# Kernel optimization log

Measured on AMD Instinct MI355X. Metric: run time of the kernel, lower is better.

Reference implementation:

```python
import jax, jax.numpy as jnp
import numpy as np

B, T, N, H, D = 8, 128, 170, 4, 16
F = H * D  # 64
LN_EPS = 1e-5
MASK_FILL = -(2.0 ** 15) + 1.0  # -32767, matches torch code


def setup_inputs() -> dict:
    key = jax.random.key(0)
    ks = jax.random.split(key, 16)
    s = 0.05
    def w(k):
        return jax.random.normal(k, (F, F), jnp.float32) * s
    def b(k):
        return jax.random.normal(k, (F,), jnp.float32) * s
    return {
        "x": jax.random.normal(ks[0], (B, T, N, F), jnp.float32),
        "te": jax.random.normal(ks[1], (B, T, N, F), jnp.float32),
        "Wq": w(ks[2]), "bq": b(ks[3]),
        "Wk": w(ks[4]), "bk": b(ks[5]),
        "Wv": w(ks[6]), "bv": b(ks[7]),
        "Wo": w(ks[8]), "bo": b(ks[9]),
        "Wf1": w(ks[10]), "bf1": b(ks[11]),
        "Wf2": w(ks[12]), "bf2": b(ks[13]),
    }


def _ln(v):
    # LayerNorm over last dim, elementwise_affine=False
    m = jnp.mean(v, axis=-1, keepdims=True)
    var = jnp.mean((v - m) ** 2, axis=-1, keepdims=True)
    return (v - m) / jnp.sqrt(var + LN_EPS)


def reference(x, te, Wq, bq, Wk, bk, Wv, bv, Wo, bo, Wf1, bf1, Wf2, bf2):
    x = x + te  # [B,T,N,F]
    # q/k/v projections (FeedForward with L=1 -> plain linear, no ReLU)
    q = (x @ Wq + bq).reshape(B, T, N, H, D)
    k = (x @ Wk + bk).reshape(B, T, N, H, D)
    v = (x @ Wv + bv).reshape(B, T, N, H, D)
    # attention over time axis, independent per node n and head h
    att = jnp.einsum('btnhd,bsnhd->bhnts', q, k) / jnp.sqrt(jnp.float32(D))
    causal = jnp.tril(jnp.ones((T, T), dtype=bool))  # keep s <= t
    att = jnp.where(causal[None, None, None, :, :], att, MASK_FILL)
    att = jax.nn.softmax(att, axis=-1)
    out = jnp.einsum('bhnts,bsnhd->btnhd', att, v).reshape(B, T, N, F)
    out = out @ Wo + bo  # ofc
    val = _ln(out + x)
    # ff: Linear-ReLU-Linear with residual + LN (res_ln=True)
    ff = jax.nn.relu(val @ Wf1 + bf1) @ Wf2 + bf2
    return _ln(ff + val)
```

## Files before the change

kernel.cpp:

```cpp
#include <hip/hip_runtime.h>

typedef __attribute__((ext_vector_type(8))) short short8;
typedef __attribute__((ext_vector_type(4))) float f32x4;
typedef __attribute__((ext_vector_type(16))) float f32x16;

#define B_ 8
#define T_ 128
#define N_ 170
#define F_ 64
#define ROWSTRIDE (N_ * F_)

union U4 { unsigned u[4]; short8 s; };

__device__ __forceinline__ unsigned short f2bf(float f) {
    union { float f; unsigned u; } v; v.f = f;
    unsigned r = v.u + 0x7fffu + ((v.u >> 16) & 1u);
    return (unsigned short)(r >> 16);
}
__device__ __forceinline__ unsigned cvtpk(float lo, float hi) {
    unsigned d;
    asm("v_cvt_pk_bf16_f32 %0, %1, %2" : "=v"(d) : "v"(lo), "v"(hi));
    return d;
}
__device__ __forceinline__ int swz128(int row, int byteInRow) {
    return row * 128 + (byteInRow ^ ((row & 7) << 4));
}
__device__ __forceinline__ int swz256(int row, int byteInRow) {
    return row * 256 + (byteInRow ^ ((row & 15) << 4));
}
__device__ __forceinline__ short8 ldfrag16(const char* base, int row0, int kbyte, int lane) {
    int row = row0 + (lane & 15);
    return *(const short8*)(base + swz128(row, kbyte + ((lane >> 4) << 4)));
}
__device__ __forceinline__ short8 ldfrag16w(const char* base, int row0, int kbyte, int lane) {
    int row = row0 + (lane & 15);
    return *(const short8*)(base + swz256(row, kbyte + ((lane >> 4) << 4)));
}
__device__ __forceinline__ short8 ldfrag32(const char* base, int row0, int colbyte, int lane) {
    int row = row0 + (lane & 31);
    return *(const short8*)(base + swz128(row, colbyte + ((lane >> 5) << 4)));
}
__device__ __forceinline__ short8 wfragT(const unsigned short* __restrict__ wT, int nt, int kc, int lane) {
    int j  = nt * 16 + (lane & 15);
    int k0 = kc * 32 + ((lane >> 4) & 3) * 8;
    return *(const short8*)(wT + j * 64 + k0);
}
__device__ __forceinline__ f32x4 zero4() {
    f32x4 v = {0.f, 0.f, 0.f, 0.f};
    return v;
}
__device__ __forceinline__ f32x16 zero16() {
    f32x16 v = {0.f, 0.f, 0.f, 0.f, 0.f, 0.f, 0.f, 0.f,
                0.f, 0.f, 0.f, 0.f, 0.f, 0.f, 0.f, 0.f};
    return v;
}

__device__ __forceinline__ void ln64(const float (&z)[2][4][4], float (&o)[2][4][4]) {
#pragma unroll
    for (int mi = 0; mi < 2; ++mi)
#pragma unroll
    for (int r = 0; r < 4; ++r) {
        float s = z[mi][0][r] + z[mi][1][r] + z[mi][2][r] + z[mi][3][r];
        s += __shfl_xor(s, 1); s += __shfl_xor(s, 2);
        s += __shfl_xor(s, 4); s += __shfl_xor(s, 8);
        float mean = s * 0.015625f;
        float d[4]; float q = 0.f;
#pragma unroll
        for (int nt = 0; nt < 4; ++nt) { d[nt] = z[mi][nt][r] - mean; q += d[nt] * d[nt]; }
        q += __shfl_xor(q, 1); q += __shfl_xor(q, 2);
        q += __shfl_xor(q, 4); q += __shfl_xor(q, 8);
        float rstd = __builtin_amdgcn_rsqf(q * 0.015625f + 1e-5f);
#pragma unroll
        for (int nt = 0; nt < 4; ++nt) o[mi][nt][r] = d[nt] * rstd;
    }
}

__global__ void prep_weights(const float* __restrict__ Wq, const float* __restrict__ Wk,
                             const float* __restrict__ Wv, const float* __restrict__ Wo,
                             const float* __restrict__ Wf1, const float* __restrict__ Wf2,
                             unsigned short* __restrict__ ws) {
    const float* Ws[6] = {Wq, Wk, Wv, Wo, Wf1, Wf2};
    const float* W = Ws[blockIdx.x];
    unsigned short* o = ws + blockIdx.x * 4096;
#pragma unroll
    for (int i = 0; i < 16; ++i) {
        int idx = i * 256 + threadIdx.x;
        int j = idx >> 6, k = idx & 63;
        o[idx] = f2bf(W[k * 64 + j]);
    }
}

__global__ __launch_bounds__(256, 3)
void ta_fused(const float* __restrict__ x, const float* __restrict__ te,
              const unsigned short* __restrict__ wT,
              const float* __restrict__ bq, const float* __restrict__ bk,
              const float* __restrict__ bv, const float* __restrict__ bo,
              const float* __restrict__ bf1, const float* __restrict__ bf2,
              float* __restrict__ out)
{
    __shared__ __align__(16) char sKb[16384];
    __shared__ __align__(16) char sVt[16384];
    __shared__ __align__(16) char sBn[16384];

    const int tid  = threadIdx.x;
    const int lane = tid & 63;
    const int wv   = tid >> 6;
    const int lam  = lane & 15;
    const int g    = (lane >> 4) & 3;
    const int bid  = blockIdx.x;
    const int b    = bid / N_;
    const int n    = bid - b * N_;
    const long long base = ((long long)b * T_ * N_ + n) * F_;
    const int t0w = wv * 32;
    char* myb = sBn + wv * 4096;

    short8 ax[2][2];
#pragma unroll
    for (int mi = 0; mi < 2; ++mi) {
        const float* xr = x  + base + (long long)(t0w + mi * 16 + lam) * ROWSTRIDE;
        const float* tr = te + base + (long long)(t0w + mi * 16 + lam) * ROWSTRIDE;
#pragma unroll
        for (int kc = 0; kc < 2; ++kc) {
            int f0 = kc * 32 + g * 8;
            float4 a0 = *(const float4*)(xr + f0);
            float4 a1 = *(const float4*)(xr + f0 + 4);
            float4 c0 = *(const float4*)(tr + f0);
            float4 c1 = *(const float4*)(tr + f0 + 4);
            U4 u;
            u.u[0] = cvtpk(a0.x + c0.x, a0.y + c0.y);
            u.u[1] = cvtpk(a0.z + c0.z, a0.w + c0.w);
            u.u[2] = cvtpk(a1.x + c1.x, a1.y + c1.y);
            u.u[3] = cvtpk(a1.z + c1.z, a1.w + c1.w);
            ax[mi][kc] = u.s;
        }
    }

    {
        const float* bp[3] = {bq, bk, bv};
#pragma unroll
        for (int w = 0; w < 3; ++w) {
            const unsigned short* wTp = wT + w * 4096;
            short8 bw[4][2]; float bias[4];
#pragma unroll
            for (int nt = 0; nt < 4; ++nt) {
                bw[nt][0] = wfragT(wTp, nt, 0, lane);
                bw[nt][1] = wfragT(wTp, nt, 1, lane);
                bias[nt]  = bp[w][nt * 16 + lam];
            }
            f32x4 acc[2][4];
#pragma unroll
            for (int mi = 0; mi < 2; ++mi)
#pragma unroll
            for (int nt = 0; nt < 4; ++nt) acc[mi][nt] = zero4();
#pragma unroll
            for (int kc = 0; kc < 2; ++kc)
#pragma unroll
            for (int mi = 0; mi < 2; ++mi)
#pragma unroll
            for (int nt = 0; nt < 4; ++nt)
                acc[mi][nt] = __builtin_amdgcn_mfma_f32_16x16x32_bf16(ax[mi][kc], bw[nt][kc], acc[mi][nt], 0, 0, 0);

            if (w == 0) {
#pragma unroll
                for (int mi = 0; mi < 2; ++mi)
#pragma unroll
                for (int nt = 0; nt < 4; ++nt)
#pragma unroll
                for (int r = 0; r < 4; ++r) {
                    int t = mi * 16 + g * 4 + r;
                    int f = nt * 16 + lam;
                    *(unsigned short*)(myb + swz128(t, f * 2)) = f2bf(acc[mi][nt][r] + bias[nt]);
                }
            } else if (w == 1) {
#pragma unroll
                for (int mi = 0; mi < 2; ++mi)
#pragma unroll
                for (int nt = 0; nt < 4; ++nt)
#pragma unroll
                for (int r = 0; r < 4; ++r) {
                    int t = t0w + mi * 16 + g * 4 + r;
                    int f = nt * 16 + lam;
                    *(unsigned short*)(sKb + swz128(t, f * 2)) = f2bf(acc[mi][nt][r] + bias[nt]);
                }
            } else {
#pragma unroll
                for (int mi = 0; mi < 2; ++mi)
#pragma unroll
                for (int nt = 0; nt < 4; ++nt) {
                    int f   = nt * 16 + lam;
                    int tb0 = t0w + mi * 16 + g * 4;
                    unsigned d0 = cvtpk(acc[mi][nt][0] + bias[nt], acc[mi][nt][1] + bias[nt]);
                    unsigned d1 = cvtpk(acc[mi][nt][2] + bias[nt], acc[mi][nt][3] + bias[nt]);
                    unsigned long long pkv = (unsigned long long)d0 | ((unsigned long long)d1 << 32);
                    *(unsigned long long*)(sVt + swz256(f, tb0 * 2)) = pkv;
                }
            }
        }
    }
    __syncthreads();

    {
        const int tcol = lane & 31;
        const int hi4  = (lane >> 5) * 4;
        f32x4 oacc[4][2];
#pragma unroll
        for (int h = 0; h < 4; ++h) { oacc[h][0] = zero4(); oacc[h][1] = zero4(); }

#pragma unroll
        for (int h = 0; h < 4; ++h) {
            short8 qf = ldfrag32(myb, 0, h * 32, lane);
            f32x16 sacc[4];
#pragma unroll
            for (int sb = 0; sb < 4; ++sb) {
                if (sb > wv) continue;
                short8 kf = ldfrag32(sKb, sb * 32, h * 32, lane);
                sacc[sb] = __builtin_amdgcn_mfma_f32_32x32x16_bf16(kf, qf, zero16(), 0, 0, 0);
                if (sb == wv) {
#pragma unroll
                    for (int r = 0; r < 16; ++r) {
                        int srow = (r & 3) + 8 * (r >> 2) + hi4;
                        if (srow > tcol) sacc[sb][r] = -3.0e38f;
                    }
                }
            }
            float m = -3.0e38f;
#pragma unroll
            for (int sb = 0; sb < 4; ++sb) {
                if (sb > wv) continue;
#pragma unroll
                for (int r = 0; r < 16; ++r) m = fmaxf(m, sacc[sb][r]);
            }
            m = fmaxf(m, __shfl_xor(m, 32));
            float sum = 0.f;
#pragma unroll
            for (int sb = 0; sb < 4; ++sb) {
                if (sb > wv) continue;
#pragma unroll
                for (int r = 0; r < 16; ++r) {
                    float p = __expf((sacc[sb][r] - m) * 0.25f);
                    sacc[sb][r] = p; sum += p;
                }
            }
            sum += __shfl_xor(sum, 32);
            float rs = __builtin_amdgcn_rcpf(sum);

#pragma unroll
            for (int sb = 0; sb < 4; ++sb) {
                if (sb > wv) continue;
                float ps[16];
#pragma unroll
                for (int r = 0; r < 16; ++r) ps[r] = sacc[sb][r] * rs;
                unsigned a0 = cvtpk(ps[0],  ps[1]);
                unsigned a1 = cvtpk(ps[4],  ps[5]);
                unsigned a2 = cvtpk(ps[8],  ps[9]);
                unsigned a3 = cvtpk(ps[12], ps[13]);
                unsigned b0 = cvtpk(ps[2],  ps[3]);
                unsigned b1 = cvtpk(ps[6],  ps[7]);
                unsigned b2 = cvtpk(ps[10], ps[11]);
                unsigned b3 = cvtpk(ps[14], ps[15]);
                asm("v_permlane32_swap_b32 %0, %1" : "+v"(a0), "+v"(a2));
                asm("v_permlane32_swap_b32 %0, %1" : "+v"(a1), "+v"(a3));
                asm("v_permlane16_swap_b32 %0, %1" : "+v"(a0), "+v"(a1));
                asm("v_permlane16_swap_b32 %0, %1" : "+v"(a2), "+v"(a3));
                asm("v_permlane32_swap_b32 %0, %1" : "+v"(b0), "+v"(b2));
                asm("v_permlane32_swap_b32 %0, %1" : "+v"(b1), "+v"(b3));
                asm("v_permlane16_swap_b32 %0, %1" : "+v"(b0), "+v"(b1));
                asm("v_permlane16_swap_b32 %0, %1" : "+v"(b2), "+v"(b3));
                U4 F0, F1;
                F0.u[0] = a0; F0.u[1] = b0; F0.u[2] = a2; F0.u[3] = b2;
                F1.u[0] = a1; F1.u[1] = b1; F1.u[2] = a3; F1.u[3] = b3;
                short8 vf = ldfrag16w(sVt, h * 16, sb * 64, lane);
                oacc[h][0] = __builtin_amdgcn_mfma_f32_16x16x32_bf16(F0.s, vf, oacc[h][0], 0, 0, 0);
                oacc[h][1] = __builtin_amdgcn_mfma_f32_16x16x32_bf16(F1.s, vf, oacc[h][1], 0, 0, 0);
            }
        }

#pragma unroll
        for (int h = 0; h < 4; ++h)
#pragma unroll
        for (int mi = 0; mi < 2; ++mi)
#pragma unroll
        for (int r = 0; r < 4; ++r) {
            int t = mi * 16 + g * 4 + r;
            int f = h * 16 + lam;
            *(unsigned short*)(myb + swz128(t, f * 2)) = f2bf(oacc[h][mi][r]);
        }
    }

    float val[2][4][4];
    {
        short8 af[2][2];
#pragma unroll
        for (int mi = 0; mi < 2; ++mi)
#pragma unroll
        for (int kc = 0; kc < 2; ++kc) af[mi][kc] = ldfrag16(myb, mi * 16, kc * 64, lane);
        const unsigned short* wTp = wT + 3 * 4096;
        short8 bwf[4][2]; float bias[4];
#pragma unroll
        for (int nt = 0; nt < 4; ++nt) {
            bwf[nt][0] = wfragT(wTp, nt, 0, lane);
            bwf[nt][1] = wfragT(wTp, nt, 1, lane);
            bias[nt]   = bo[nt * 16 + lam];
        }
        f32x4 acc[2][4];
#pragma unroll
        for (int mi = 0; mi < 2; ++mi)
#pragma unroll
        for (int nt = 0; nt < 4; ++nt) acc[mi][nt] = zero4();
#pragma unroll
        for (int kc = 0; kc < 2; ++kc)
#pragma unroll
        for (int mi = 0; mi < 2; ++mi)
#pragma unroll
        for (int nt = 0; nt < 4; ++nt)
            acc[mi][nt] = __builtin_amdgcn_mfma_f32_16x16x32_bf16(af[mi][kc], bwf[nt][kc], acc[mi][nt], 0, 0, 0);
        float z[2][4][4];
#pragma unroll
        for (int mi = 0; mi < 2; ++mi)
#pragma unroll
        for (int nt = 0; nt < 4; ++nt)
#pragma unroll
        for (int r = 0; r < 4; ++r) {
            long long off = base + (long long)(t0w + mi * 16 + g * 4 + r) * ROWSTRIDE + nt * 16 + lam;
            z[mi][nt][r] = acc[mi][nt][r] + bias[nt] + x[off] + te[off];
        }
        ln64(z, val);
#pragma unroll
        for (int mi = 0; mi < 2; ++mi)
#pragma unroll
        for (int nt = 0; nt < 4; ++nt)
#pragma unroll
        for (int r = 0; r < 4; ++r) {
            int t = mi * 16 + g * 4 + r;
            int f = nt * 16 + lam;
            *(unsigned short*)(myb + swz128(t, f * 2)) = f2bf(val[mi][nt][r]);
        }
    }

    {
        short8 af[2][2];
#pragma unroll
        for (int mi = 0; mi < 2; ++mi)
#pragma unroll
        for (int kc = 0; kc < 2; ++kc) af[mi][kc] = ldfrag16(myb, mi * 16, kc * 64, lane);
        const unsigned short* wTp = wT + 4 * 4096;
        short8 bwf[4][2]; float bias[4];
#pragma unroll
        for (int nt = 0; nt < 4; ++nt) {
            bwf[nt][0] = wfragT(wTp, nt, 0, lane);
            bwf[nt][1] = wfragT(wTp, nt, 1, lane);
            bias[nt]   = bf1[nt * 16 + lam];
        }
        f32x4 acc[2][4];
#pragma unroll
        for (int mi = 0; mi < 2; ++mi)
#pragma unroll
        for (int nt = 0; nt < 4; ++nt) acc[mi][nt] = zero4();
#pragma unroll
        for (int kc = 0; kc < 2; ++kc)
#pragma unroll
        for (int mi = 0; mi < 2; ++mi)
#pragma unroll
        for (int nt = 0; nt < 4; ++nt)
            acc[mi][nt] = __builtin_amdgcn_mfma_f32_16x16x32_bf16(af[mi][kc], bwf[nt][kc], acc[mi][nt], 0, 0, 0);
#pragma unroll
        for (int mi = 0; mi < 2; ++mi)
#pragma unroll
        for (int nt = 0; nt < 4; ++nt)
#pragma unroll
        for (int r = 0; r < 4; ++r) {
            int t = mi * 16 + g * 4 + r;
            int f = nt * 16 + lam;
            *(unsigned short*)(myb + swz128(t, f * 2)) = f2bf(fmaxf(acc[mi][nt][r] + bias[nt], 0.f));
        }
    }

    {
        short8 af[2][2];
#pragma unroll
        for (int mi = 0; mi < 2; ++mi)
#pragma unroll
        for (int kc = 0; kc < 2; ++kc) af[mi][kc] = ldfrag16(myb, mi * 16, kc * 64, lane);
        const unsigned short* wTp = wT + 5 * 4096;
        short8 bwf[4][2]; float bias[4];
#pragma unroll
        for (int nt = 0; nt < 4; ++nt) {
            bwf[nt][0] = wfragT(wTp, nt, 0, lane);
            bwf[nt][1] = wfragT(wTp, nt, 1, lane);
            bias[nt]   = bf2[nt * 16 + lam];
        }
        f32x4 acc[2][4];
#pragma unroll
        for (int mi = 0; mi < 2; ++mi)
#pragma unroll
        for (int nt = 0; nt < 4; ++nt) acc[mi][nt] = zero4();
#pragma unroll
        for (int kc = 0; kc < 2; ++kc)
#pragma unroll
        for (int mi = 0; mi < 2; ++mi)
#pragma unroll
        for (int nt = 0; nt < 4; ++nt)
            acc[mi][nt] = __builtin_amdgcn_mfma_f32_16x16x32_bf16(af[mi][kc], bwf[nt][kc], acc[mi][nt], 0, 0, 0);
        float z[2][4][4], res[2][4][4];
#pragma unroll
        for (int mi = 0; mi < 2; ++mi)
#pragma unroll
        for (int nt = 0; nt < 4; ++nt)
#pragma unroll
        for (int r = 0; r < 4; ++r)
            z[mi][nt][r] = acc[mi][nt][r] + bias[nt] + val[mi][nt][r];
        ln64(z, res);
#pragma unroll
        for (int mi = 0; mi < 2; ++mi)
#pragma unroll
        for (int nt = 0; nt < 4; ++nt)
#pragma unroll
        for (int r = 0; r < 4; ++r) {
            int t = t0w + mi * 16 + g * 4 + r;
            int f = nt * 16 + lam;
            out[base + (long long)t * ROWSTRIDE + f] = res[mi][nt][r];
        }
    }
}

extern "C" void kernel_launch(void* const* d_in, const int* in_sizes, int n_in,
                              void* d_out, int out_size, void* d_ws, size_t ws_size,
                              hipStream_t stream) {
    const float* x   = (const float*)d_in[0];
    const float* te  = (const float*)d_in[1];
    const float* Wq  = (const float*)d_in[2];
    const float* bq  = (const float*)d_in[3];
    const float* Wk  = (const float*)d_in[4];
    const float* bk  = (const float*)d_in[5];
    const float* Wv  = (const float*)d_in[6];
    const float* bv  = (const float*)d_in[7];
    const float* Wo  = (const float*)d_in[8];
    const float* bo  = (const float*)d_in[9];
    const float* Wf1 = (const float*)d_in[10];
    const float* bf1 = (const float*)d_in[11];
    const float* Wf2 = (const float*)d_in[12];
    const float* bf2 = (const float*)d_in[13];
    unsigned short* wsT = (unsigned short*)d_ws;

    prep_weights<<<dim3(6), dim3(256), 0, stream>>>(Wq, Wk, Wv, Wo, Wf1, Wf2, wsT);
    ta_fused<<<dim3(B_ * N_), dim3(256), 0, stream>>>(
        x, te, wsT, bq, bk, bv, bo, bf1, bf2, (float*)d_out);
}
```

Baseline: 73.37 us.

## Swap MFMA operands so accumulators hold contiguous features per lane

Swaps the A/B operands of the projection, output and feed-forward MFMAs so each lane's accumulator holds four consecutive feature columns of one row instead of four rows of one column. This lets the kernel write packed 64-bit bf16 values to LDS, load biases and residuals as float4, store the output as float4, and reduce LayerNorm with two cross-lane shuffles instead of four per row. The goal is fewer scalar LDS and global accesses and fewer shuffles. The swizzled LDS layouts must still line up with the fragment loaders used downstream.

```diff
diff --git a/kernel.cpp b/kernel.cpp
--- a/kernel.cpp
+++ b/kernel.cpp
@@ -55,23 +55,27 @@
     return v;
 }
 
-__device__ __forceinline__ void ln64(const float (&z)[2][4][4], float (&o)[2][4][4]) {
-#pragma unroll
-    for (int mi = 0; mi < 2; ++mi)
-#pragma unroll
-    for (int r = 0; r < 4; ++r) {
-        float s = z[mi][0][r] + z[mi][1][r] + z[mi][2][r] + z[mi][3][r];
-        s += __shfl_xor(s, 1); s += __shfl_xor(s, 2);
-        s += __shfl_xor(s, 4); s += __shfl_xor(s, 8);
+__device__ __forceinline__ void lnS(float (&z)[2][4][4]) {
+#pragma unroll
+    for (int mi = 0; mi < 2; ++mi) {
+        float s = 0.f;
+#pragma unroll
+        for (int nt = 0; nt < 4; ++nt)
+#pragma unroll
+        for (int r = 0; r < 4; ++r) s += z[mi][nt][r];
+        s += __shfl_xor(s, 16); s += __shfl_xor(s, 32);
         float mean = s * 0.015625f;
-        float d[4]; float q = 0.f;
-#pragma unroll
-        for (int nt = 0; nt < 4; ++nt) { d[nt] = z[mi][nt][r] - mean; q += d[nt] * d[nt]; }
-        q += __shfl_xor(q, 1); q += __shfl_xor(q, 2);
-        q += __shfl_xor(q, 4); q += __shfl_xor(q, 8);
+        float q = 0.f;
+#pragma unroll
+        for (int nt = 0; nt < 4; ++nt)
+#pragma unroll
+        for (int r = 0; r < 4; ++r) { z[mi][nt][r] -= mean; q += z[mi][nt][r] * z[mi][nt][r]; }
+        q += __shfl_xor(q, 16); q += __shfl_xor(q, 32);
         float rstd = __builtin_amdgcn_rsqf(q * 0.015625f + 1e-5f);
 #pragma unroll
-        for (int nt = 0; nt < 4; ++nt) o[mi][nt][r] = d[nt] * rstd;
+        for (int nt = 0; nt < 4; ++nt)
+#pragma unroll
+        for (int r = 0; r < 4; ++r) z[mi][nt][r] *= rstd;
     }
 }
 
@@ -136,53 +140,57 @@
     }
 
     {
-        const float* bp[3] = {bq, bk, bv};
 #pragma unroll
         for (int w = 0; w < 3; ++w) {
             const unsigned short* wTp = wT + w * 4096;
-            short8 bw[4][2]; float bias[4];
+            short8 bw[4][2];
 #pragma unroll
             for (int nt = 0; nt < 4; ++nt) {
                 bw[nt][0] = wfragT(wTp, nt, 0, lane);
                 bw[nt][1] = wfragT(wTp, nt, 1, lane);
-                bias[nt]  = bp[w][nt * 16 + lam];
             }
             f32x4 acc[2][4];
 #pragma unroll
             for (int mi = 0; mi < 2; ++mi)
 #pragma unroll
             for (int nt = 0; nt < 4; ++nt) acc[mi][nt] = zero4();
-#pragma unroll
-            for (int kc = 0; kc < 2; ++kc)
-#pragma unroll
-            for (int mi = 0; mi < 2; ++mi)
-#pragma unroll
-            for (int nt = 0; nt < 4; ++nt)
-                acc[mi][nt] = __builtin_amdgcn_mfma_f32_16x16x32_bf16(ax[mi][kc], bw[nt][kc], acc[mi][nt], 0, 0, 0);
-
-            if (w == 0) {
+
+            if (w < 2) {
+                const float* bp = (w == 0) ? bq : bk;
+                float4 bj[4];
+#pragma unroll
+                for (int nt = 0; nt < 4; ++nt) bj[nt] = *(const float4*)(bp + nt * 16 + g * 4);
+#pragma unroll
+                for (int kc = 0; kc < 2; ++kc)
 #pragma unroll
                 for (int mi = 0; mi < 2; ++mi)
 #pragma unroll
                 for (int nt = 0; nt < 4; ++nt)
-#pragma unroll
-                for (int r = 0; r < 4; ++r) {
-                    int t = mi * 16 + g * 4 + r;
-                    int f = nt * 16 + lam;
-                    *(unsigned short*)(myb + swz128(t, f * 2)) = f2bf(acc[mi][nt][r] + bias[nt]);
-                }
-            } else if (w == 1) {
+                    acc[mi][nt] = __builtin_amdgcn_mfma_f32_16x16x32_bf16(bw[nt][kc], ax[mi][kc], acc[mi][nt], 0, 0, 0);
 #pragma unroll
                 for (int mi = 0; mi < 2; ++mi)
 #pragma unroll
-                for (int nt = 0; nt < 4; ++nt)
-#pragma unroll
-                for (int r = 0; r < 4; ++r) {
-                    int t = t0w + mi * 16 + g * 4 + r;
-                    int f = nt * 16 + lam;
-                    *(unsigned short*)(sKb + swz128(t, f * 2)) = f2bf(acc[mi][nt][r] + bias[nt]);
+                for (int nt = 0; nt < 4; ++nt) {
+                    unsigned d0 = cvtpk(acc[mi][nt][0] + bj[nt].x, acc[mi][nt][1] + bj[nt].y);
+                    unsigned d1 = cvtpk(acc[mi][nt][2] + bj[nt].z, acc[mi][nt][3] + bj[nt].w);
+                    unsigned long long pk = (unsigned long long)d0 | ((unsigned long long)d1 << 32);
+                    if (w == 0) {
+                        *(unsigned long long*)(myb + swz128(mi * 16 + lam, (nt * 16 + g * 4) * 2)) = pk;
+                    } else {
+                        *(unsigned long long*)(sKb + swz128(t0w + mi * 16 + lam, (nt * 16 + g * 4) * 2)) = pk;
+                    }
                 }
             } else {
+                float bias[4];
+#pragma unroll
+                for (int nt = 0; nt < 4; ++nt) bias[nt] = bv[nt * 16 + lam];
+#pragma unroll
+                for (int kc = 0; kc < 2; ++kc)
+#pragma unroll
+                for (int mi = 0; mi < 2; ++mi)
+#pragma unroll
+                for (int nt = 0; nt < 4; ++nt)
+                    acc[mi][nt] = __builtin_amdgcn_mfma_f32_16x16x32_bf16(ax[mi][kc], bw[nt][kc], acc[mi][nt], 0, 0, 0);
 #pragma unroll
                 for (int mi = 0; mi < 2; ++mi)
 #pragma unroll
@@ -202,9 +210,9 @@
     {
         const int tcol = lane & 31;
         const int hi4  = (lane >> 5) * 4;
-        f32x4 oacc[4][2];
-#pragma unroll
-        for (int h = 0; h < 4; ++h) { oacc[h][0] = zero4(); oacc[h][1] = zero4(); }
+        f32x4 oaccT[4][2];
+#pragma unroll
+        for (int h = 0; h < 4; ++h) { oaccT[h][0] = zero4(); oaccT[h][1] = zero4(); }
 
 #pragma unroll
         for (int h = 0; h < 4; ++h) {
@@ -270,20 +278,19 @@
                 F0.u[0] = a0; F0.u[1] = b0; F0.u[2] = a2; F0.u[3] = b2;
                 F1.u[0] = a1; F1.u[1] = b1; F1.u[2] = a3; F1.u[3] = b3;
                 short8 vf = ldfrag16w(sVt, h * 16, sb * 64, lane);
-                oacc[h][0] = __builtin_amdgcn_mfma_f32_16x16x32_bf16(F0.s, vf, oacc[h][0], 0, 0, 0);
-                oacc[h][1] = __builtin_amdgcn_mfma_f32_16x16x32_bf16(F1.s, vf, oacc[h][1], 0, 0, 0);
+                oaccT[h][0] = __builtin_amdgcn_mfma_f32_16x16x32_bf16(vf, F0.s, oaccT[h][0], 0, 0, 0);
+                oaccT[h][1] = __builtin_amdgcn_mfma_f32_16x16x32_bf16(vf, F1.s, oaccT[h][1], 0, 0, 0);
             }
         }
 
 #pragma unroll
         for (int h = 0; h < 4; ++h)
 #pragma unroll
-        for (int mi = 0; mi < 2; ++mi)
-#pragma unroll
-        for (int r = 0; r < 4; ++r) {
-            int t = mi * 16 + g * 4 + r;
-            int f = h * 16 + lam;
-            *(unsigned short*)(myb + swz128(t, f * 2)) = f2bf(oacc[h][mi][r]);
+        for (int mi = 0; mi < 2; ++mi) {
+            unsigned d0 = cvtpk(oaccT[h][mi][0], oaccT[h][mi][1]);
+            unsigned d1 = cvtpk(oaccT[h][mi][2], oaccT[h][mi][3]);
+            unsigned long long pk = (unsigned long long)d0 | ((unsigned long long)d1 << 32);
+            *(unsigned long long*)(myb + swz128(mi * 16 + lam, (h * 16 + g * 4) * 2)) = pk;
         }
     }
 
@@ -295,12 +302,12 @@
 #pragma unroll
         for (int kc = 0; kc < 2; ++kc) af[mi][kc] = ldfrag16(myb, mi * 16, kc * 64, lane);
         const unsigned short* wTp = wT + 3 * 4096;
-        short8 bwf[4][2]; float bias[4];
+        short8 bwf[4][2]; float4 bj[4];
 #pragma unroll
         for (int nt = 0; nt < 4; ++nt) {
             bwf[nt][0] = wfragT(wTp, nt, 0, lane);
             bwf[nt][1] = wfragT(wTp, nt, 1, lane);
-            bias[nt]   = bo[nt * 16 + lam];
+            bj[nt]     = *(const float4*)(bo + nt * 16 + g * 4);
         }
         f32x4 acc[2][4];
 #pragma unroll
@@ -313,27 +320,28 @@
         for (int mi = 0; mi < 2; ++mi)
 #pragma unroll
         for (int nt = 0; nt < 4; ++nt)
-            acc[mi][nt] = __builtin_amdgcn_mfma_f32_16x16x32_bf16(af[mi][kc], bwf[nt][kc], acc[mi][nt], 0, 0, 0);
-        float z[2][4][4];
-#pragma unroll
-        for (int mi = 0; mi < 2; ++mi)
-#pragma unroll
-        for (int nt = 0; nt < 4; ++nt)
-#pragma unroll
-        for (int r = 0; r < 4; ++r) {
-            long long off = base + (long long)(t0w + mi * 16 + g * 4 + r) * ROWSTRIDE + nt * 16 + lam;
-            z[mi][nt][r] = acc[mi][nt][r] + bias[nt] + x[off] + te[off];
-        }
-        ln64(z, val);
-#pragma unroll
-        for (int mi = 0; mi < 2; ++mi)
-#pragma unroll
-        for (int nt = 0; nt < 4; ++nt)
-#pragma unroll
-        for (int r = 0; r < 4; ++r) {
-            int t = mi * 16 + g * 4 + r;
-            int f = nt * 16 + lam;
-            *(unsigned short*)(myb + swz128(t, f * 2)) = f2bf(val[mi][nt][r]);
+            acc[mi][nt] = __builtin_amdgcn_mfma_f32_16x16x32_bf16(bwf[nt][kc], af[mi][kc], acc[mi][nt], 0, 0, 0);
+#pragma unroll
+        for (int mi = 0; mi < 2; ++mi)
+#pragma unroll
+        for (int nt = 0; nt < 4; ++nt) {
+            long long roff = base + (long long)(t0w + mi * 16 + lam) * ROWSTRIDE + nt * 16 + g * 4;
+            float4 xv = *(const float4*)(x + roff);
+            float4 tv = *(const float4*)(te + roff);
+            val[mi][nt][0] = acc[mi][nt][0] + bj[nt].x + xv.x + tv.x;
+            val[mi][nt][1] = acc[mi][nt][1] + bj[nt].y + xv.y + tv.y;
+            val[mi][nt][2] = acc[mi][nt][2] + bj[nt].z + xv.z + tv.z;
+            val[mi][nt][3] = acc[mi][nt][3] + bj[nt].w + xv.w + tv.w;
+        }
+        lnS(val);
+#pragma unroll
+        for (int mi = 0; mi < 2; ++mi)
+#pragma unroll
+        for (int nt = 0; nt < 4; ++nt) {
+            unsigned d0 = cvtpk(val[mi][nt][0], val[mi][nt][1]);
+            unsigned d1 = cvtpk(val[mi][nt][2], val[mi][nt][3]);
+            unsigned long long pk = (unsigned long long)d0 | ((unsigned long long)d1 << 32);
+            *(unsigned long long*)(myb + swz128(mi * 16 + lam, (nt * 16 + g * 4) * 2)) = pk;
         }
     }
 
@@ -344,12 +352,12 @@
 #pragma unroll
         for (int kc = 0; kc < 2; ++kc) af[mi][kc] = ldfrag16(myb, mi * 16, kc * 64, lane);
         const unsigned short* wTp = wT + 4 * 4096;
-        short8 bwf[4][2]; float bias[4];
+        short8 bwf[4][2]; float4 bj[4];
 #pragma unroll
         for (int nt = 0; nt < 4; ++nt) {
             bwf[nt][0] = wfragT(wTp, nt, 0, lane);
             bwf[nt][1] = wfragT(wTp, nt, 1, lane);
-            bias[nt]   = bf1[nt * 16 + lam];
+            bj[nt]     = *(const float4*)(bf1 + nt * 16 + g * 4);
         }
         f32x4 acc[2][4];
 #pragma unroll
@@ -362,16 +370,15 @@
         for (int mi = 0; mi < 2; ++mi)
 #pragma unroll
         for (int nt = 0; nt < 4; ++nt)
-            acc[mi][nt] = __builtin_amdgcn_mfma_f32_16x16x32_bf16(af[mi][kc], bwf[nt][kc], acc[mi][nt], 0, 0, 0);
-#pragma unroll
-        for (int mi = 0; mi < 2; ++mi)
-#pragma unroll
-        for (int nt = 0; nt < 4; ++nt)
-#pragma unroll
-        for (int r = 0; r < 4; ++r) {
-            int t = mi * 16 + g * 4 + r;
-            int f = nt * 16 + lam;
-            *(unsigned short*)(myb + swz128(t, f * 2)) = f2bf(fmaxf(acc[mi][nt][r] + bias[nt], 0.f));
+            acc[mi][nt] = __builtin_amdgcn_mfma_f32_16x16x32_bf16(bwf[nt][kc], af[mi][kc], acc[mi][nt], 0, 0, 0);
+#pragma unroll
+        for (int mi = 0; mi < 2; ++mi)
+#pragma unroll
+        for (int nt = 0; nt < 4; ++nt) {
+            unsigned d0 = cvtpk(fmaxf(acc[mi][nt][0] + bj[nt].x, 0.f), fmaxf(acc[mi][nt][1] + bj[nt].y, 0.f));
+            unsigned d1 = cvtpk(fmaxf(acc[mi][nt][2] + bj[nt].z, 0.f), fmaxf(acc[mi][nt][3] + bj[nt].w, 0.f));
+            unsigned long long pk = (unsigned long long)d0 | ((unsigned long long)d1 << 32);
+            *(unsigned long long*)(myb + swz128(mi * 16 + lam, (nt * 16 + g * 4) * 2)) = pk;
         }
     }
 
@@ -382,12 +389,12 @@
 #pragma unroll
         for (int kc = 0; kc < 2; ++kc) af[mi][kc] = ldfrag16(myb, mi * 16, kc * 64, lane);
         const unsigned short* wTp = wT + 5 * 4096;
-        short8 bwf[4][2]; float bias[4];
+        short8 bwf[4][2]; float4 bj[4];
 #pragma unroll
         for (int nt = 0; nt < 4; ++nt) {
             bwf[nt][0] = wfragT(wTp, nt, 0, lane);
             bwf[nt][1] = wfragT(wTp, nt, 1, lane);
-            bias[nt]   = bf2[nt * 16 + lam];
+            bj[nt]     = *(const float4*)(bf2 + nt * 16 + g * 4);
         }
         f32x4 acc[2][4];
 #pragma unroll
@@ -400,25 +407,24 @@
         for (int mi = 0; mi < 2; ++mi)
 #pragma unroll
         for (int nt = 0; nt < 4; ++nt)
-            acc[mi][nt] = __builtin_amdgcn_mfma_f32_16x16x32_bf16(af[mi][kc], bwf[nt][kc], acc[mi][nt], 0, 0, 0);
-        float z[2][4][4], res[2][4][4];
-#pragma unroll
-        for (int mi = 0; mi < 2; ++mi)
-#pragma unroll
-        for (int nt = 0; nt < 4; ++nt)
-#pragma unroll
-        for (int r = 0; r < 4; ++r)
-            z[mi][nt][r] = acc[mi][nt][r] + bias[nt] + val[mi][nt][r];
-        ln64(z, res);
-#pragma unroll
-        for (int mi = 0; mi < 2; ++mi)
-#pragma unroll
-        for (int nt = 0; nt < 4; ++nt)
-#pragma unroll
-        for (int r = 0; r < 4; ++r) {
-            int t = t0w + mi * 16 + g * 4 + r;
-            int f = nt * 16 + lam;
-            out[base + (long long)t * ROWSTRIDE + f] = res[mi][nt][r];
+            acc[mi][nt] = __builtin_amdgcn_mfma_f32_16x16x32_bf16(bwf[nt][kc], af[mi][kc], acc[mi][nt], 0, 0, 0);
+        float z[2][4][4];
+#pragma unroll
+        for (int mi = 0; mi < 2; ++mi)
+#pragma unroll
+        for (int nt = 0; nt < 4; ++nt) {
+            z[mi][nt][0] = acc[mi][nt][0] + bj[nt].x + val[mi][nt][0];
+            z[mi][nt][1] = acc[mi][nt][1] + bj[nt].y + val[mi][nt][1];
+            z[mi][nt][2] = acc[mi][nt][2] + bj[nt].z + val[mi][nt][2];
+            z[mi][nt][3] = acc[mi][nt][3] + bj[nt].w + val[mi][nt][3];
+        }
+        lnS(z);
+#pragma unroll
+        for (int mi = 0; mi < 2; ++mi)
+#pragma unroll
+        for (int nt = 0; nt < 4; ++nt) {
+            float4 o = {z[mi][nt][0], z[mi][nt][1], z[mi][nt][2], z[mi][nt][3]};
+            *(float4*)(out + base + (long long)(t0w + mi * 16 + lam) * ROWSTRIDE + nt * 16 + g * 4) = o;
         }
     }
 }
```

Result: no change. 74.22 us (+1.2%).
